# Performance work log

Hardware: AMD Instinct MI355X
Metric: run time of the kernel (lower is better)

The kernel has to match this reference:

```python
import jax, jax.numpy as jnp
import numpy as np

B, N, E, D, H = 128, 256, 1024, 128, 8
DK = D // H
NEG = -9e15

def _xavier(key, shape):
    lim = np.sqrt(6.0 / (shape[0] + shape[1]))
    return jax.random.uniform(key, shape, jnp.float32, -lim, lim)

def setup_inputs() -> dict:
    key = jax.random.key(0)
    ks = jax.random.split(key, 10)
    x = jax.random.normal(ks[0], (B, N, D), jnp.float32)
    mask = jax.random.randint(ks[1], (B, N), 0, 2) > 0
    mask = mask.at[:, 0].set(True)  # ensure no fully-masked molecule
    # unique (row, col) edges per molecule -> scatter .set matches torch index_put
    perm = jax.vmap(lambda k: jax.random.permutation(k, N * N)[:E])(jax.random.split(ks[2], B))
    edge_index = jnp.stack([perm // N, perm % N], axis=1).astype(jnp.int32)  # [B, 2, E]
    edge_attr = jax.random.normal(ks[3], (B, E, D), jnp.float32)
    return {
        "x": x, "mask": mask, "edge_index": edge_index, "edge_attr": edge_attr,
        "Wq": _xavier(ks[4], (D + 2, D)),
        "Wk": _xavier(ks[5], (D + 2, D)),
        "Wv": _xavier(ks[6], (D + 2, D)),
        "We_w": _xavier(ks[7], (D, D)),
        "We_b": jax.random.normal(ks[8], (D,), jnp.float32) * 0.02,
        "ln_g": jnp.ones((D,), jnp.float32),
        "ln_b": jnp.zeros((D,), jnp.float32),
    }

def reference(x, mask, edge_index, edge_attr, Wq, Wk, Wv, We_w, We_b, ln_g, ln_b):
    rows, cols = edge_index[:, 0, :], edge_index[:, 1, :]  # [B, E]
    # per-molecule degree features (torch_geometric.degree per row/col)
    deg = lambda idx: jax.vmap(lambda r: jnp.zeros((N,), x.dtype).at[r].add(1.0))(idx)
    deg_r, deg_c = deg(rows), deg(cols)
    x_new = jnp.concatenate([x, deg_r[..., None], deg_c[..., None]], axis=-1)  # [B,N,D+2]
    # edge bias: linear -> mean over features -> scatter into [B,N,N]
    edge_feats = (edge_attr @ We_w + We_b).mean(axis=-1)  # [B, E]
    edge_bias = jax.vmap(lambda r, c, f: jnp.zeros((N, N), x.dtype).at[r, c].set(f))(rows, cols, edge_feats)
    q = (x_new @ Wq).reshape(B, N, H, DK).transpose(0, 2, 1, 3)
    k = (x_new @ Wk).reshape(B, N, H, DK).transpose(0, 2, 1, 3)
    v = (x_new @ Wv).reshape(B, N, H, DK).transpose(0, 2, 1, 3)
    scores = jnp.einsum('bhqd,bhkd->bhqk', q, k) / np.sqrt(DK).astype(x.dtype)
    # mask keys first, then add edge bias (matches torch op order)
    scores = jnp.where(mask[:, None, None, :], scores, NEG) + edge_bias[:, None, :, :]
    attn = jax.nn.softmax(scores, axis=-1)  # dropout is identity in eval
    out = jnp.einsum('bhqk,bhkd->bhqd', attn, v).transpose(0, 2, 1, 3).reshape(B, N, D)
    out = out + x
    mu = out.mean(axis=-1, keepdims=True)
    var = out.var(axis=-1, keepdims=True)
    return (out - mu) / jnp.sqrt(var + 1e-6) * ln_g + ln_b
```

## Files before the change

### kernel.cpp

```cpp
#include <hip/hip_runtime.h>
#include <stdint.h>

#define NB 128
#define NN 256
#define NE 1024
#define ND 128
#define NH 8
#define NDK 16
#define NEGV -9.0e15f

typedef unsigned short u16;
typedef unsigned int u32;
typedef unsigned char u8;
typedef __attribute__((ext_vector_type(8))) short short8;
typedef __attribute__((ext_vector_type(4))) float float4v;
typedef __attribute__((ext_vector_type(2))) float f32x2;

__device__ __forceinline__ float bf2f(u16 u) { return __uint_as_float(((u32)u) << 16); }
__device__ __forceinline__ u16 f2bf(float f) {
    u32 u = __float_as_uint(f);
    u += 0x7fffu + ((u >> 16) & 1u);
    return (u16)(u >> 16);
}
__device__ __forceinline__ float ldf(const void* p, size_t i, int f32) {
    return f32 ? ((const float*)p)[i] : bf2f(((const u16*)p)[i]);
}
__device__ __forceinline__ void stf(void* p, size_t i, int f32, float v) {
    if (f32) ((float*)p)[i] = v;
    else ((u16*)p)[i] = f2bf(v);
}
__device__ __forceinline__ void unpack8(uint4 a, float* o) {
    o[0] = bf2f(a.x & 0xffff); o[1] = bf2f(a.x >> 16);
    o[2] = bf2f(a.y & 0xffff); o[3] = bf2f(a.y >> 16);
    o[4] = bf2f(a.z & 0xffff); o[5] = bf2f(a.z >> 16);
    o[6] = bf2f(a.w & 0xffff); o[7] = bf2f(a.w >> 16);
}
__device__ __forceinline__ f32x2 bfpair(u32 w) {
    return (f32x2){__uint_as_float(w << 16), __uint_as_float(w & 0xffff0000u)};
}
__device__ __forceinline__ u32 pk_bf(float a, float b) {
    return ((__float_as_uint(a) + 0x8000u) >> 16) |
           ((__float_as_uint(b) + 0x8000u) & 0xffff0000u);
}
union Pack8 { u16 u[8]; u32 w[4]; short8 v; };

__global__ __launch_bounds__(256) void k_detect(const u16* x16, const u8* m8, int* flags) {
    __shared__ u32 sev[256], sg1[256], smx[256];
    int tid = threadIdx.x;
    u32 ev = 0;
    const uint4* xv = (const uint4*)(x16 + tid * 128);
#pragma unroll
    for (int i = 0; i < 16; ++i) {
        uint4 a = xv[i];
        u32 w[4] = {a.x, a.y, a.z, a.w};
#pragma unroll
        for (int j = 0; j < 4; ++j) {
            ev |= ((((w[j] & 0xffffu) >> 7) & 0xffu) >= 0xC2u) ? 1u : 0u;
            ev |= ((((w[j] >> 16) >> 7) & 0xffu) >= 0xC2u) ? 1u : 0u;
        }
    }
    u32 g1 = 0, mx = 0;
    {
        uint4 m = *(const uint4*)(m8 + tid * 16);
        u32 w[4] = {m.x, m.y, m.z, m.w};
#pragma unroll
        for (int j = 0; j < 4; ++j) {
            u32 b0 = w[j] & 0xffu, b1 = (w[j] >> 8) & 0xffu;
            u32 b2 = (w[j] >> 16) & 0xffu, b3 = w[j] >> 24;
            g1 |= b1;
            u32 ma = b0 > b1 ? b0 : b1, mbv = b2 > b3 ? b2 : b3;
            u32 mc = ma > mbv ? ma : mbv;
            mx = mx > mc ? mx : mc;
        }
    }
    sev[tid] = ev; sg1[tid] = g1; smx[tid] = mx;
    __syncthreads();
    for (int s = 128; s > 0; s >>= 1) {
        if (tid < s) {
            sev[tid] |= sev[tid + s];
            sg1[tid] |= sg1[tid + s];
            smx[tid] = smx[tid] > smx[tid + s] ? smx[tid] : smx[tid + s];
        }
        __syncthreads();
    }
    if (tid == 0) {
        flags[0] = sev[0] ? 1 : 0;
        flags[1] = (sg1[0] == 0) ? 4 : ((smx[0] <= 1u) ? 1 : 2);
    }
}

__global__ __launch_bounds__(64) void k_wmean(const void* Wew, const void* Web,
                                              const int* flags, float* wmean) {
    int k = blockIdx.x, lane = threadIdx.x;
    int f32 = flags[0];
    const void* src = (k < 128) ? Wew : Web;
    size_t base = (k < 128) ? (size_t)k * ND : 0;
    float s = ldf(src, base + lane, f32) + ldf(src, base + lane + 64, f32);
#pragma unroll
    for (int off = 32; off; off >>= 1) s += __shfl_xor(s, off, 64);
    if (lane == 0) wmean[k] = s * (1.0f / ND);
}

__global__ __launch_bounds__(256) void k_efeat(const void* ea, const float* wmean,
                                               const int* flags, float* featsE) {
    __shared__ __align__(16) float swm[132];
    int tid = threadIdx.x;
    int f32 = flags[0];
    if (tid <= ND) swm[tid] = wmean[tid];
    __syncthreads();
    int sub = tid & 15, grp = tid >> 4;
    size_t eidx = (size_t)blockIdx.x * 16 + grp;
    const float4* wv = (const float4*)&swm[sub * 8];
    float4 w0 = wv[0], w1 = wv[1];
    size_t base = eidx * ND + sub * 8;
    float part;
    if (f32) {
        const float4* p = (const float4*)((const float*)ea + base);
        float4 a0 = p[0], a1 = p[1];
        part = a0.x * w0.x + a0.y * w0.y + a0.z * w0.z + a0.w * w0.w +
               a1.x * w1.x + a1.y * w1.y + a1.z * w1.z + a1.w * w1.w;
    } else {
        uint4 a = *(const uint4*)((const u16*)ea + base);
        float xv[8];
        unpack8(a, xv);
        part = xv[0] * w0.x + xv[1] * w0.y + xv[2] * w0.z + xv[3] * w0.w +
               xv[4] * w1.x + xv[5] * w1.y + xv[6] * w1.z + xv[7] * w1.w;
    }
    part += __shfl_xor(part, 1);
    part += __shfl_xor(part, 2);
    part += __shfl_xor(part, 4);
    part += __shfl_xor(part, 8);
    if (sub == 0) featsE[eidx] = part + swm[ND];
}

__global__ __launch_bounds__(256) void k_csr(const int* ei, const float* featsE,
                                             float* degr, float* degc, int* rowstartG,
                                             u16* colsG, float* featsG) {
    __shared__ int cr[NN], cc[NN], offs[NN], rs[NN + 1];
    int b = blockIdx.x, tid = threadIdx.x;
    cr[tid] = 0; cc[tid] = 0;
    __syncthreads();
    const int* rows = ei + (size_t)b * 2 * NE;
    const int* cols = rows + NE;
    for (int e = tid; e < NE; e += 256) {
        atomicAdd(&cr[rows[e]], 1);
        atomicAdd(&cc[cols[e]], 1);
    }
    __syncthreads();
    degr[b * NN + tid] = (float)cr[tid];
    degc[b * NN + tid] = (float)cc[tid];
    if (tid == 0) {
        int a = 0;
        for (int n = 0; n < NN; ++n) { rs[n] = a; a += cr[n]; }
        rs[NN] = a;
    }
    __syncthreads();
    offs[tid] = rs[tid];
    rowstartG[b * (NN + 1) + tid] = rs[tid];
    if (tid == 0) rowstartG[b * (NN + 1) + NN] = rs[NN];
    __syncthreads();
    for (int e = tid; e < NE; e += 256) {
        int r = rows[e];
        int pos = atomicAdd(&offs[r], 1);
        colsG[(size_t)b * NE + pos] = (u16)cols[e];
        featsG[(size_t)b * NE + pos] = featsE[(size_t)b * NE + e];
    }
}

__global__ __launch_bounds__(64) void k_packB(const void* Wq, const void* Wk,
                                              const void* Wv, const int* flags, u16* WP) {
    int kT = blockIdx.x / 24, nT = blockIdx.x % 24;
    int lane = threadIdx.x;
    int col = lane & 15, quad = lane >> 4;
    int n = nT * 16 + col;
    int mat = n >> 7, nm = n & 127;
    const void* W = (mat == 0) ? Wq : (mat == 1) ? Wk : Wv;
    int f32 = flags[0];
    Pack8 c;
#pragma unroll
    for (int j = 0; j < 8; ++j) {
        int k = kT * 32 + quad * 8 + j;
        c.u[j] = (k < 130) ? f2bf(ldf(W, (size_t)k * ND + nm, f32)) : (u16)0;
    }
    *(short8*)(WP + ((size_t)(kT * 24 + nT) * 64 + lane) * 8) = c.v;
}

__global__ __launch_bounds__(256) void k_gemm(const void* x, const float* degr,
                                              const float* degc, const u16* WP,
                                              const int* flags, u16* qw, u16* kw,
                                              u16* vw, u16* vt) {
    int tid = threadIdx.x;
    int w = tid >> 6, lane = tid & 63;
    int quad = lane >> 4, col = lane & 15;
    int m0 = blockIdx.x * 64 + w * 16;
    int row = m0 + col;
    int f32 = flags[0];

    float4v acc[24];
#pragma unroll
    for (int t = 0; t < 24; ++t) acc[t] = (float4v){0.f, 0.f, 0.f, 0.f};

    const short8* wp = (const short8*)WP;
    for (int kT = 0; kT < 5; ++kT) {
        short8 a;
        if (kT < 4) {
            if (!f32) {
                a = *(const short8*)((const u16*)x + (size_t)row * ND + kT * 32 + quad * 8);
            } else {
                const float* xf = (const float*)x + (size_t)row * ND + kT * 32 + quad * 8;
                Pack8 c;
#pragma unroll
                for (int j = 0; j < 8; ++j) c.u[j] = f2bf(xf[j]);
                a = c.v;
            }
        } else {
            Pack8 c;
#pragma unroll
            for (int j = 0; j < 8; ++j) c.u[j] = 0;
            if (quad == 0) {
                c.u[0] = f2bf(degr[row]);
                c.u[1] = f2bf(degc[row]);
            }
            a = c.v;
        }
#pragma unroll
        for (int nT = 0; nT < 24; ++nT) {
            short8 bfr = wp[(size_t)(kT * 24 + nT) * 64 + lane];
            acc[nT] = __builtin_amdgcn_mfma_f32_16x16x32_bf16(a, bfr, acc[nT], 0, 0, 0);
        }
    }
    int bb = m0 >> 8;
    int nodebase = (m0 & 255) + quad * 4;
#pragma unroll
    for (int nT = 0; nT < 16; ++nT) {
        int h = nT & 7;
        u16* O = (nT < 8) ? qw : kw;
        float sc = (nT < 8) ? 0.25f : 1.0f;
        size_t base = ((size_t)bb * NH + h) * NN + nodebase;
#pragma unroll
        for (int reg = 0; reg < 4; ++reg)
            O[(base + reg) * NDK + col] = f2bf(acc[nT][reg] * sc);
    }
#pragma unroll
    for (int nT = 16; nT < 24; ++nT) {
        int h = nT - 16;
        size_t base = ((size_t)bb * NH + h) * NN + nodebase;
#pragma unroll
        for (int reg = 0; reg < 4; ++reg)
            vw[(base + reg) * NDK + col] = f2bf(acc[nT][reg]);
        u32 lo = (u32)f2bf(acc[nT][0]) | ((u32)f2bf(acc[nT][1]) << 16);
        u32 hi = (u32)f2bf(acc[nT][2]) | ((u32)f2bf(acc[nT][3]) << 16);
        *(uint2*)(vt + (((size_t)bb * NH + h) * NDK + col) * NN + nodebase) = make_uint2(lo, hi);
    }
}

__global__ __launch_bounds__(256, 4) void k_attn(const u16* qg, const u16* kg,
                                              const u16* vw, const u16* vt,
                                              const void* mask, const int* flags,
                                              const int* rowstartG, const u16* colsG,
                                              const float* featsG, void* out) {
    __shared__ __align__(16) u16 Ks[NN][24];
    __shared__ __align__(16) u16 Vs[NDK][264];
    __shared__ __align__(16) float mb[NN];
    __shared__ __align__(16) float Of[NN * 17];
    __shared__ float lbuf[NN];
    int h = blockIdx.x, b = blockIdx.y, tid = threadIdx.x;
    int wv = tid >> 6, lane = tid & 63;
    int col = lane & 15, g = lane >> 4;
    int f32 = flags[0], mw = flags[1];
    size_t hb = ((size_t)b * NH + h) * NN;
    int e0 = rowstartG[b * (NN + 1) + tid];
    int e1 = rowstartG[b * (NN + 1) + tid + 1];
    const uint4* ksrc = (const uint4*)(kg + (hb + tid) * NDK);
    uint4 ka0 = ksrc[0], ka1 = ksrc[1];
    int dk = tid >> 4, chunk = tid & 15;
    const uint4* vsrc = (const uint4*)(vt + ((size_t)(b * NH + h) * NDK + dk) * NN + chunk * 16);
    uint4 va0 = vsrc[0], va1 = vsrc[1];
    bool mv;
    {
        size_t mi = (size_t)b * NN + tid;
        if (mw == 4)      mv = ((const u32*)mask)[mi] != 0;
        else if (mw == 2) mv = ((const u16*)mask)[mi] != 0;
        else              mv = ((const u8*)mask)[mi] != 0;
    }
    f32x2 qr[8];
    {
        const uint4* qp = (const uint4*)(qg + (hb + tid) * NDK);
        uint4 qa_ = qp[0], qb_ = qp[1];
        qr[0] = bfpair(qa_.x); qr[1] = bfpair(qa_.y);
        qr[2] = bfpair(qa_.z); qr[3] = bfpair(qa_.w);
        qr[4] = bfpair(qb_.x); qr[5] = bfpair(qb_.y);
        qr[6] = bfpair(qb_.z); qr[7] = bfpair(qb_.w);
    }
    short8 qf[4];
#pragma unroll
    for (int qt = 0; qt < 4; ++qt) {
        int qtabs = wv * 4 + qt;
        short8 qv = {0, 0, 0, 0, 0, 0, 0, 0};
        if (g < 2)
            qv = *(const short8*)(qg + (hb + qtabs * 16 + col) * NDK + 8 * g);
        qf[qt] = qv;
    }
    {
        uint4* kdst = (uint4*)&Ks[tid][0];
        kdst[0] = ka0; kdst[1] = ka1;
        uint4* vdst = (uint4*)&Vs[dk][chunk * 16];
        vdst[0] = va0; vdst[1] = va1;
        mb[tid] = mv ? 0.0f : NEGV;
    }
    __syncthreads();

    float4v outv[4];
    float lpart[4];
#pragma unroll
    for (int qt = 0; qt < 4; ++qt) {
        outv[qt] = (float4v){0.f, 0.f, 0.f, 0.f};
        lpart[qt] = 0.f;
    }

    for (int kt = 0; kt < 16; ++kt) {
        short8 kf = {0, 0, 0, 0, 0, 0, 0, 0};
        if (g < 2) kf = *(const short8*)&Ks[kt * 16 + col][8 * g];
        Pack8 vv;
        {
            uint2 t2 = *(const uint2*)&Vs[col][kt * 16 + 4 * g];
            vv.w[0] = t2.x; vv.w[1] = t2.y; vv.w[2] = 0; vv.w[3] = 0;
        }
        float4 mb4 = *(const float4*)&mb[kt * 16 + 4 * g];
        float4v cin = (float4v){mb4.x, mb4.y, mb4.z, mb4.w};
#pragma unroll
        for (int qt = 0; qt < 4; ++qt) {
            float4v s4 = __builtin_amdgcn_mfma_f32_16x16x32_bf16(kf, qf[qt], cin, 0, 0, 0);
            float p0 = __expf(fminf(s4[0], 60.f));
            float p1 = __expf(fminf(s4[1], 60.f));
            float p2 = __expf(fminf(s4[2], 60.f));
            float p3 = __expf(fminf(s4[3], 60.f));
            lpart[qt] += (p0 + p1) + (p2 + p3);
            Pack8 pp;
            pp.w[0] = pk_bf(p0, p1);
            pp.w[1] = pk_bf(p2, p3);
            pp.w[2] = 0; pp.w[3] = 0;
            outv[qt] = __builtin_amdgcn_mfma_f32_16x16x32_bf16(pp.v, vv.v, outv[qt], 0, 0, 0);
        }
    }
#pragma unroll
    for (int qt = 0; qt < 4; ++qt) {
        float l = lpart[qt];
        l += __shfl_xor(l, 16);
        l += __shfl_xor(l, 32);
        if (g == 0) lbuf[(wv * 4 + qt) * 16 + col] = l;
        int q0 = (wv * 4 + qt) * 16 + 4 * g;
#pragma unroll
        for (int reg = 0; reg < 4; ++reg)
            Of[(q0 + reg) * 17 + col] = outv[qt][reg];
    }
    __syncthreads();

    float lfin = lbuf[tid];
    f32x2 r[8];
#pragma unroll
    for (int j = 0; j < 8; ++j)
        r[j] = (f32x2){Of[tid * 17 + 2 * j], Of[tid * 17 + 2 * j + 1]};
    if (e0 < e1) {
        const u16* colsB = colsG + (size_t)b * NE;
        const float* featsB = featsG + (size_t)b * NE;
        int c = colsB[e0];
        float f = featsB[e0];
        const uint4* vp0 = (const uint4*)(vw + (hb + c) * NDK);
        uint4 v0 = vp0[0], v1 = vp0[1];
        for (int e = e0; e < e1; ++e) {
            int cc_ = c; float ff_ = f;
            uint4 w0 = v0, w1 = v1;
            if (e + 1 < e1) {
                c = colsB[e + 1];
                f = featsB[e + 1];
                const uint4* vp = (const uint4*)(vw + (hb + c) * NDK);
                v0 = vp[0]; v1 = vp[1];
            }
            const u32* kcw = (const u32*)&Ks[cc_][0];
            f32x2 s2 = qr[0] * bfpair(kcw[0]);
            s2 += qr[1] * bfpair(kcw[1]); s2 += qr[2] * bfpair(kcw[2]);
            s2 += qr[3] * bfpair(kcw[3]); s2 += qr[4] * bfpair(kcw[4]);
            s2 += qr[5] * bfpair(kcw[5]); s2 += qr[6] * bfpair(kcw[6]);
            s2 += qr[7] * bfpair(kcw[7]);
            float s = s2.x + s2.y + mb[cc_];
            float dl = __expf(fminf(s + ff_, 60.f)) - __expf(fminf(s, 60.f));
            lfin += dl;
            f32x2 d2 = (f32x2){dl, dl};
            r[0] += d2 * bfpair(w0.x); r[1] += d2 * bfpair(w0.y);
            r[2] += d2 * bfpair(w0.z); r[3] += d2 * bfpair(w0.w);
            r[4] += d2 * bfpair(w1.x); r[5] += d2 * bfpair(w1.y);
            r[6] += d2 * bfpair(w1.z); r[7] += d2 * bfpair(w1.w);
        }
    }
    float inv = 1.0f / lfin;
    size_t obase = ((size_t)(b * NN + tid)) * ND + h * NDK;
    if (f32) {
        float4* op = (float4*)((float*)out + obase);
#pragma unroll
        for (int jj = 0; jj < 4; ++jj) {
            float4 w;
            w.x = r[2 * jj].x * inv;     w.y = r[2 * jj].y * inv;
            w.z = r[2 * jj + 1].x * inv; w.w = r[2 * jj + 1].y * inv;
            op[jj] = w;
        }
    } else {
        u16* op = (u16*)out + obase;
        Pack8 pa, pb;
#pragma unroll
        for (int jj = 0; jj < 4; ++jj) {
            pa.u[2 * jj]     = f2bf(r[jj].x * inv);
            pa.u[2 * jj + 1] = f2bf(r[jj].y * inv);
            pb.u[2 * jj]     = f2bf(r[jj + 4].x * inv);
            pb.u[2 * jj + 1] = f2bf(r[jj + 4].y * inv);
        }
        *(uint4*)op = *(uint4*)&pa.w[0];
        *(uint4*)(op + 8) = *(uint4*)&pb.w[0];
    }
}

__global__ __launch_bounds__(256) void k_ln(void* out, const void* x, const void* g,
                                            const void* be, const int* flags) {
    int f32 = flags[0];
    int tid = threadIdx.x, wv = tid >> 6, lane = tid & 63;
    int row = blockIdx.x * 4 + wv;
    size_t base = (size_t)row * ND;
    float v0 = ldf(out, base + lane, f32) + ldf(x, base + lane, f32);
    float v1 = ldf(out, base + lane + 64, f32) + ldf(x, base + lane + 64, f32);
    float s = v0 + v1, ss = v0 * v0 + v1 * v1;
#pragma unroll
    for (int off = 32; off; off >>= 1) {
        s += __shfl_xor(s, off, 64);
        ss += __shfl_xor(ss, off, 64);
    }
    float mu = s * (1.0f / ND);
    float var = ss * (1.0f / ND) - mu * mu;
    float rs = rsqrtf(var + 1e-6f);
    float o0 = (v0 - mu) * rs * ldf(g, lane, f32) + ldf(be, lane, f32);
    float o1 = (v1 - mu) * rs * ldf(g, lane + 64, f32) + ldf(be, lane + 64, f32);
    stf(out, base + lane, f32, o0);
    stf(out, base + lane + 64, f32, o1);
}

extern "C" void kernel_launch(void* const* d_in, const int* in_sizes, int n_in,
                              void* d_out, int out_size, void* d_ws, size_t ws_size,
                              hipStream_t stream) {
    const void* x = d_in[0];
    const void* mask = d_in[1];
    const int* ei = (const int*)d_in[2];
    const void* ea = d_in[3];
    const void* Wq = d_in[4];
    const void* Wk = d_in[5];
    const void* Wv = d_in[6];
    const void* Wew = d_in[7];
    const void* Web = d_in[8];
    const void* lng = d_in[9];
    const void* lnb = d_in[10];

    char* ws = (char*)d_ws;
    size_t off = 0;
    int* flags = (int*)(ws + off);       off += 256;
    float* wmean = (float*)(ws + off);   off += 1024;
    float* degr = (float*)(ws + off);    off += (size_t)NB * NN * 4;
    float* degc = (float*)(ws + off);    off += (size_t)NB * NN * 4;
    int* rowstart = (int*)(ws + off);    off += (size_t)NB * (NN + 1) * 4 + 512;
    u16* colsG = (u16*)(ws + off);       off += (size_t)NB * NE * 2;
    float* featsG = (float*)(ws + off);  off += (size_t)NB * NE * 4;
    float* featsE = (float*)(ws + off);  off += (size_t)NB * NE * 4;
    u16* WP = (u16*)(ws + off);          off += (size_t)5 * 24 * 64 * 8 * 2;
    const size_t qkv_elems = (size_t)NB * NH * NN * NDK;
    u16* qw = (u16*)(ws + off);          off += qkv_elems * 2;
    u16* kw = (u16*)(ws + off);          off += qkv_elems * 2;
    u16* vw = (u16*)(ws + off);          off += qkv_elems * 2;
    u16* vt = (u16*)(ws + off);          off += qkv_elems * 2;

    k_detect<<<1, 256, 0, stream>>>((const u16*)x, (const u8*)mask, flags);
    k_wmean<<<129, 64, 0, stream>>>(Wew, Web, flags, wmean);
    k_efeat<<<(NB * NE) / 16, 256, 0, stream>>>(ea, wmean, flags, featsE);
    k_csr<<<NB, 256, 0, stream>>>(ei, featsE, degr, degc, rowstart, colsG, featsG);
    k_packB<<<120, 64, 0, stream>>>(Wq, Wk, Wv, flags, WP);
    k_gemm<<<(NB * NN) / 64, 256, 0, stream>>>(x, degr, degc, WP, flags, qw, kw, vw, vt);
    k_attn<<<dim3(NH, NB), 256, 0, stream>>>(qw, kw, vw, vt, mask, flags, rowstart,
                                             colsG, featsG, d_out);
    k_ln<<<(NB * NN) / 4, 256, 0, stream>>>(d_out, x, lng, lnb, flags);
}
```

Before: 209.5 us.

## Fuse preprocessing kernels and detect dtype per wave instead of via flags

Removes the single-block detect kernel and its flags buffer. Each kernel now does a cheap per-wave dtype/mask-format probe on a small slice of x and mask. The wmean and weight-packing kernels are merged into one launch. Edge-feature computation is folded into the CSR kernel using shared memory, which removes the featsE global round trip and cuts the launch count from 8 to 5. In exchange, the per-molecule edge projection now runs on only 128 blocks (one per molecule), so that phase has less parallelism. The dtype probe also checks far fewer elements than before, which may be less robust.

```diff
diff --git a/kernel.cpp b/kernel.cpp
--- a/kernel.cpp
+++ b/kernel.cpp
@@ -44,102 +44,118 @@
 }
 union Pack8 { u16 u[8]; u32 w[4]; short8 v; };
 
-__global__ __launch_bounds__(256) void k_detect(const u16* x16, const u8* m8, int* flags) {
-    __shared__ u32 sev[256], sg1[256], smx[256];
-    int tid = threadIdx.x;
+__device__ __forceinline__ int wave_detect_f32(const u16* x16) {
+    int lane = threadIdx.x & 63;
+    uint4 a = *(const uint4*)(x16 + lane * 8);
+    u32 w[4] = {a.x, a.y, a.z, a.w};
     u32 ev = 0;
-    const uint4* xv = (const uint4*)(x16 + tid * 128);
-#pragma unroll
-    for (int i = 0; i < 16; ++i) {
-        uint4 a = xv[i];
-        u32 w[4] = {a.x, a.y, a.z, a.w};
-#pragma unroll
-        for (int j = 0; j < 4; ++j) {
-            ev |= ((((w[j] & 0xffffu) >> 7) & 0xffu) >= 0xC2u) ? 1u : 0u;
-            ev |= ((((w[j] >> 16) >> 7) & 0xffu) >= 0xC2u) ? 1u : 0u;
-        }
-    }
+#pragma unroll
+    for (int j = 0; j < 4; ++j) {
+        ev |= ((((w[j] & 0xffffu) >> 7) & 0xffu) >= 0xC2u) ? 1u : 0u;
+        ev |= (((w[j] >> 23) & 0xffu) >= 0xC2u) ? 1u : 0u;
+    }
+#pragma unroll
+    for (int off = 32; off; off >>= 1) ev |= (u32)__shfl_xor((int)ev, off, 64);
+    return ev ? 1 : 0;
+}
+__device__ __forceinline__ int wave_detect_mw(const u8* m8) {
+    int lane = threadIdx.x & 63;
+    uint4 m = *(const uint4*)(m8 + lane * 16);
+    u32 w[4] = {m.x, m.y, m.z, m.w};
     u32 g1 = 0, mx = 0;
-    {
-        uint4 m = *(const uint4*)(m8 + tid * 16);
-        u32 w[4] = {m.x, m.y, m.z, m.w};
-#pragma unroll
-        for (int j = 0; j < 4; ++j) {
-            u32 b0 = w[j] & 0xffu, b1 = (w[j] >> 8) & 0xffu;
-            u32 b2 = (w[j] >> 16) & 0xffu, b3 = w[j] >> 24;
-            g1 |= b1;
-            u32 ma = b0 > b1 ? b0 : b1, mbv = b2 > b3 ? b2 : b3;
-            u32 mc = ma > mbv ? ma : mbv;
-            mx = mx > mc ? mx : mc;
-        }
-    }
-    sev[tid] = ev; sg1[tid] = g1; smx[tid] = mx;
-    __syncthreads();
-    for (int s = 128; s > 0; s >>= 1) {
-        if (tid < s) {
-            sev[tid] |= sev[tid + s];
-            sg1[tid] |= sg1[tid + s];
-            smx[tid] = smx[tid] > smx[tid + s] ? smx[tid] : smx[tid + s];
-        }
-        __syncthreads();
-    }
-    if (tid == 0) {
-        flags[0] = sev[0] ? 1 : 0;
-        flags[1] = (sg1[0] == 0) ? 4 : ((smx[0] <= 1u) ? 1 : 2);
-    }
-}
-
-__global__ __launch_bounds__(64) void k_wmean(const void* Wew, const void* Web,
-                                              const int* flags, float* wmean) {
-    int k = blockIdx.x, lane = threadIdx.x;
-    int f32 = flags[0];
-    const void* src = (k < 128) ? Wew : Web;
-    size_t base = (k < 128) ? (size_t)k * ND : 0;
-    float s = ldf(src, base + lane, f32) + ldf(src, base + lane + 64, f32);
-#pragma unroll
-    for (int off = 32; off; off >>= 1) s += __shfl_xor(s, off, 64);
-    if (lane == 0) wmean[k] = s * (1.0f / ND);
-}
-
-__global__ __launch_bounds__(256) void k_efeat(const void* ea, const float* wmean,
-                                               const int* flags, float* featsE) {
+#pragma unroll
+    for (int j = 0; j < 4; ++j) {
+        u32 b0 = w[j] & 0xffu, b1 = (w[j] >> 8) & 0xffu;
+        u32 b2 = (w[j] >> 16) & 0xffu, b3 = w[j] >> 24;
+        g1 |= b1;
+        u32 ma = b0 > b1 ? b0 : b1, mb2 = b2 > b3 ? b2 : b3;
+        u32 mc = ma > mb2 ? ma : mb2;
+        mx = mx > mc ? mx : mc;
+    }
+#pragma unroll
+    for (int off = 32; off; off >>= 1) {
+        g1 |= (u32)__shfl_xor((int)g1, off, 64);
+        u32 o = (u32)__shfl_xor((int)mx, off, 64);
+        mx = mx > o ? mx : o;
+    }
+    return (g1 == 0) ? 4 : ((mx <= 1u) ? 1 : 2);
+}
+
+__global__ __launch_bounds__(64) void k_wpk(const u16* x16,
+                                            const void* Wew, const void* Web,
+                                            float* wmean,
+                                            const void* Wq, const void* Wk,
+                                            const void* Wv, u16* WP) {
+    int f32 = wave_detect_f32(x16);
+    int bid = blockIdx.x, lane = threadIdx.x;
+    if (bid < 129) {
+        int k = bid;
+        const void* src = (k < 128) ? Wew : Web;
+        size_t base = (k < 128) ? (size_t)k * ND : 0;
+        float s = ldf(src, base + lane, f32) + ldf(src, base + lane + 64, f32);
+#pragma unroll
+        for (int off = 32; off; off >>= 1) s += __shfl_xor(s, off, 64);
+        if (lane == 0) wmean[k] = s * (1.0f / ND);
+    } else {
+        int id = bid - 129;
+        int kT = id / 24, nT = id % 24;
+        int col = lane & 15, quad = lane >> 4;
+        int n = nT * 16 + col;
+        int mat = n >> 7, nm = n & 127;
+        const void* W = (mat == 0) ? Wq : (mat == 1) ? Wk : Wv;
+        Pack8 c;
+#pragma unroll
+        for (int j = 0; j < 8; ++j) {
+            int k = kT * 32 + quad * 8 + j;
+            c.u[j] = (k < 130) ? f2bf(ldf(W, (size_t)k * ND + nm, f32)) : (u16)0;
+        }
+        *(short8*)(WP + ((size_t)(kT * 24 + nT) * 64 + lane) * 8) = c.v;
+    }
+}
+
+__global__ __launch_bounds__(256) void k_edge(const u16* x16, const void* ea,
+                                              const float* wmean, const int* ei,
+                                              float* degr, float* degc,
+                                              int* rowstartG, u16* colsG,
+                                              float* featsG) {
     __shared__ __align__(16) float swm[132];
-    int tid = threadIdx.x;
-    int f32 = flags[0];
-    if (tid <= ND) swm[tid] = wmean[tid];
-    __syncthreads();
-    int sub = tid & 15, grp = tid >> 4;
-    size_t eidx = (size_t)blockIdx.x * 16 + grp;
-    const float4* wv = (const float4*)&swm[sub * 8];
-    float4 w0 = wv[0], w1 = wv[1];
-    size_t base = eidx * ND + sub * 8;
-    float part;
-    if (f32) {
-        const float4* p = (const float4*)((const float*)ea + base);
-        float4 a0 = p[0], a1 = p[1];
-        part = a0.x * w0.x + a0.y * w0.y + a0.z * w0.z + a0.w * w0.w +
-               a1.x * w1.x + a1.y * w1.y + a1.z * w1.z + a1.w * w1.w;
-    } else {
-        uint4 a = *(const uint4*)((const u16*)ea + base);
-        float xv[8];
-        unpack8(a, xv);
-        part = xv[0] * w0.x + xv[1] * w0.y + xv[2] * w0.z + xv[3] * w0.w +
-               xv[4] * w1.x + xv[5] * w1.y + xv[6] * w1.z + xv[7] * w1.w;
-    }
-    part += __shfl_xor(part, 1);
-    part += __shfl_xor(part, 2);
-    part += __shfl_xor(part, 4);
-    part += __shfl_xor(part, 8);
-    if (sub == 0) featsE[eidx] = part + swm[ND];
-}
-
-__global__ __launch_bounds__(256) void k_csr(const int* ei, const float* featsE,
-                                             float* degr, float* degc, int* rowstartG,
-                                             u16* colsG, float* featsG) {
+    __shared__ float featsL[NE];
     __shared__ int cr[NN], cc[NN], offs[NN], rs[NN + 1];
     int b = blockIdx.x, tid = threadIdx.x;
+    int f32 = wave_detect_f32(x16);
+    if (tid <= ND) swm[tid] = wmean[tid];
     cr[tid] = 0; cc[tid] = 0;
     __syncthreads();
+    {
+        int sub = tid & 15, grp = tid >> 4;
+        const float4* wv = (const float4*)&swm[sub * 8];
+        float4 w0 = wv[0], w1 = wv[1];
+        float wb = swm[ND];
+        const size_t ebase = (size_t)b * NE;
+#pragma unroll 4
+        for (int t = 0; t < 64; ++t) {
+            int e = t * 16 + grp;
+            size_t base = (ebase + e) * ND + sub * 8;
+            float part;
+            if (f32) {
+                const float4* p = (const float4*)((const float*)ea + base);
+                float4 a0 = p[0], a1 = p[1];
+                part = a0.x * w0.x + a0.y * w0.y + a0.z * w0.z + a0.w * w0.w +
+                       a1.x * w1.x + a1.y * w1.y + a1.z * w1.z + a1.w * w1.w;
+            } else {
+                uint4 a = *(const uint4*)((const u16*)ea + base);
+                float xv[8];
+                unpack8(a, xv);
+                part = xv[0] * w0.x + xv[1] * w0.y + xv[2] * w0.z + xv[3] * w0.w +
+                       xv[4] * w1.x + xv[5] * w1.y + xv[6] * w1.z + xv[7] * w1.w;
+            }
+            part += __shfl_xor(part, 1);
+            part += __shfl_xor(part, 2);
+            part += __shfl_xor(part, 4);
+            part += __shfl_xor(part, 8);
+            if (sub == 0) featsL[e] = part + wb;
+        }
+    }
     const int* rows = ei + (size_t)b * 2 * NE;
     const int* cols = rows + NE;
     for (int e = tid; e < NE; e += 256) {
@@ -163,38 +179,20 @@
         int r = rows[e];
         int pos = atomicAdd(&offs[r], 1);
         colsG[(size_t)b * NE + pos] = (u16)cols[e];
-        featsG[(size_t)b * NE + pos] = featsE[(size_t)b * NE + e];
-    }
-}
-
-__global__ __launch_bounds__(64) void k_packB(const void* Wq, const void* Wk,
-                                              const void* Wv, const int* flags, u16* WP) {
-    int kT = blockIdx.x / 24, nT = blockIdx.x % 24;
-    int lane = threadIdx.x;
-    int col = lane & 15, quad = lane >> 4;
-    int n = nT * 16 + col;
-    int mat = n >> 7, nm = n & 127;
-    const void* W = (mat == 0) ? Wq : (mat == 1) ? Wk : Wv;
-    int f32 = flags[0];
-    Pack8 c;
-#pragma unroll
-    for (int j = 0; j < 8; ++j) {
-        int k = kT * 32 + quad * 8 + j;
-        c.u[j] = (k < 130) ? f2bf(ldf(W, (size_t)k * ND + nm, f32)) : (u16)0;
-    }
-    *(short8*)(WP + ((size_t)(kT * 24 + nT) * 64 + lane) * 8) = c.v;
+        featsG[(size_t)b * NE + pos] = featsL[e];
+    }
 }
 
 __global__ __launch_bounds__(256) void k_gemm(const void* x, const float* degr,
                                               const float* degc, const u16* WP,
-                                              const int* flags, u16* qw, u16* kw,
+                                              u16* qw, u16* kw,
                                               u16* vw, u16* vt) {
     int tid = threadIdx.x;
     int w = tid >> 6, lane = tid & 63;
     int quad = lane >> 4, col = lane & 15;
     int m0 = blockIdx.x * 64 + w * 16;
     int row = m0 + col;
-    int f32 = flags[0];
+    int f32 = wave_detect_f32((const u16*)x);
 
     float4v acc[24];
 #pragma unroll
@@ -254,9 +252,10 @@
     }
 }
 
-__global__ __launch_bounds__(256, 4) void k_attn(const u16* qg, const u16* kg,
+__global__ __launch_bounds__(256, 4) void k_attn(const u16* x16,
+                                              const u16* qg, const u16* kg,
                                               const u16* vw, const u16* vt,
-                                              const void* mask, const int* flags,
+                                              const void* mask,
                                               const int* rowstartG, const u16* colsG,
                                               const float* featsG, void* out) {
     __shared__ __align__(16) u16 Ks[NN][24];
@@ -267,7 +266,8 @@
     int h = blockIdx.x, b = blockIdx.y, tid = threadIdx.x;
     int wv = tid >> 6, lane = tid & 63;
     int col = lane & 15, g = lane >> 4;
-    int f32 = flags[0], mw = flags[1];
+    int f32 = wave_detect_f32(x16);
+    int mw = wave_detect_mw((const u8*)mask);
     size_t hb = ((size_t)b * NH + h) * NN;
     int e0 = rowstartG[b * (NN + 1) + tid];
     int e1 = rowstartG[b * (NN + 1) + tid + 1];
@@ -420,8 +420,8 @@
 }
 
 __global__ __launch_bounds__(256) void k_ln(void* out, const void* x, const void* g,
-                                            const void* be, const int* flags) {
-    int f32 = flags[0];
+                                            const void* be) {
+    int f32 = wave_detect_f32((const u16*)x);
     int tid = threadIdx.x, wv = tid >> 6, lane = tid & 63;
     int row = blockIdx.x * 4 + wv;
     size_t base = (size_t)row * ND;
@@ -459,14 +459,12 @@
 
     char* ws = (char*)d_ws;
     size_t off = 0;
-    int* flags = (int*)(ws + off);       off += 256;
     float* wmean = (float*)(ws + off);   off += 1024;
     float* degr = (float*)(ws + off);    off += (size_t)NB * NN * 4;
     float* degc = (float*)(ws + off);    off += (size_t)NB * NN * 4;
     int* rowstart = (int*)(ws + off);    off += (size_t)NB * (NN + 1) * 4 + 512;
     u16* colsG = (u16*)(ws + off);       off += (size_t)NB * NE * 2;
     float* featsG = (float*)(ws + off);  off += (size_t)NB * NE * 4;
-    float* featsE = (float*)(ws + off);  off += (size_t)NB * NE * 4;
     u16* WP = (u16*)(ws + off);          off += (size_t)5 * 24 * 64 * 8 * 2;
     const size_t qkv_elems = (size_t)NB * NH * NN * NDK;
     u16* qw = (u16*)(ws + off);          off += qkv_elems * 2;
@@ -474,13 +472,11 @@
     u16* vw = (u16*)(ws + off);          off += qkv_elems * 2;
     u16* vt = (u16*)(ws + off);          off += qkv_elems * 2;
 
-    k_detect<<<1, 256, 0, stream>>>((const u16*)x, (const u8*)mask, flags);
-    k_wmean<<<129, 64, 0, stream>>>(Wew, Web, flags, wmean);
-    k_efeat<<<(NB * NE) / 16, 256, 0, stream>>>(ea, wmean, flags, featsE);
-    k_csr<<<NB, 256, 0, stream>>>(ei, featsE, degr, degc, rowstart, colsG, featsG);
-    k_packB<<<120, 64, 0, stream>>>(Wq, Wk, Wv, flags, WP);
-    k_gemm<<<(NB * NN) / 64, 256, 0, stream>>>(x, degr, degc, WP, flags, qw, kw, vw, vt);
-    k_attn<<<dim3(NH, NB), 256, 0, stream>>>(qw, kw, vw, vt, mask, flags, rowstart,
-                                             colsG, featsG, d_out);
-    k_ln<<<(NB * NN) / 4, 256, 0, stream>>>(d_out, x, lng, lnb, flags);
-}
+    k_wpk<<<249, 64, 0, stream>>>((const u16*)x, Wew, Web, wmean, Wq, Wk, Wv, WP);
+    k_edge<<<NB, 256, 0, stream>>>((const u16*)x, ea, wmean, ei, degr, degc,
+                                   rowstart, colsG, featsG);
+    k_gemm<<<(NB * NN) / 64, 256, 0, stream>>>(x, degr, degc, WP, qw, kw, vw, vt);
+    k_attn<<<dim3(NH, NB), 256, 0, stream>>>((const u16*)x, qw, kw, vw, vt, mask,
+                                             rowstart, colsG, featsG, d_out);
+    k_ln<<<(NB * NN) / 4, 256, 0, stream>>>(d_out, x, lng, lnb);
+}
```

Measured after the change: 241.0 us. 1.15x slower.
